# Kernel tuning notes

Measured on AMD Instinct MI355X. Metric: run time of the kernel, lower is better.

Reference implementation:

```python
import jax, jax.numpy as jnp
import numpy as np

N_NODES = 50000
N_EDGES = 800000
N_GRAPHS = 500
IN_DIM, HID, OUT = 128, 64, 10


def setup_inputs() -> dict:
    key = jax.random.key(0)
    ks = jax.random.split(key, 12)
    x = jax.random.normal(ks[0], (N_NODES, IN_DIM), dtype=jnp.float32)
    edge_index = jax.random.randint(ks[1], (2, N_EDGES), 0, N_NODES, dtype=jnp.int32)
    batch = jnp.sort(jax.random.randint(ks[2], (N_NODES,), 0, N_GRAPHS, dtype=jnp.int32))
    def glorot(k, shape):
        lim = np.sqrt(6.0 / (shape[0] + shape[1]))
        return jax.random.uniform(k, shape, jnp.float32, -lim, lim)
    return {
        "x": x, "edge_index": edge_index, "batch": batch,
        "W1": glorot(ks[3], (IN_DIM, HID)), "b1": jnp.zeros((HID,), jnp.float32),
        "W2": glorot(ks[4], (HID, HID)),    "b2": jnp.zeros((HID,), jnp.float32),
        "W3": glorot(ks[5], (HID, HID)),    "b3": jnp.zeros((HID,), jnp.float32),
        "lin_W1": glorot(ks[6], (HID, HID)), "lin_b1": jnp.zeros((HID,), jnp.float32),
        "lin_W2": glorot(ks[7], (HID, OUT)), "lin_b2": jnp.zeros((OUT,), jnp.float32),
    }


def _gcn_conv(x, src, dst, deg_inv_sqrt, W, b):
    # PyG GCNConv: h = x @ W, then sym-normalized scatter-add over edges (self-loops included in src/dst)
    h = x @ W                                   # [N, out]
    norm = deg_inv_sqrt[src] * deg_inv_sqrt[dst]  # [E+N]
    msgs = h[src] * norm[:, None]               # [E+N, out]  (large gathered intermediate)
    out = jax.ops.segment_sum(msgs, dst, num_segments=N_NODES)
    return out + b


def reference(x, edge_index, batch, W1, b1, W2, b2, W3, b3, lin_W1, lin_b1, lin_W2, lin_b2):
    # add self-loops once; degree (with edge weight 1) computed on target nodes
    loops = jnp.arange(N_NODES, dtype=edge_index.dtype)
    src = jnp.concatenate([edge_index[0], loops])
    dst = jnp.concatenate([edge_index[1], loops])
    deg = jax.ops.segment_sum(jnp.ones_like(dst, dtype=x.dtype), dst, num_segments=N_NODES)
    deg_inv_sqrt = jnp.where(deg > 0, jax.lax.rsqrt(jnp.maximum(deg, 1e-12)), 0.0)

    h = jax.nn.relu(_gcn_conv(x, src, dst, deg_inv_sqrt, W1, b1))
    h = jax.nn.relu(_gcn_conv(h, src, dst, deg_inv_sqrt, W2, b2))
    h = jax.nn.relu(_gcn_conv(h, src, dst, deg_inv_sqrt, W3, b3))

    # global mean pool over graphs
    sums = jax.ops.segment_sum(h, batch, num_segments=N_GRAPHS)
    counts = jax.ops.segment_sum(jnp.ones((h.shape[0],), h.dtype), batch, num_segments=N_GRAPHS)
    pooled = sums / jnp.maximum(counts, 1.0)[:, None]  # [G, HID]

    # MLP head (dropout p=0 / eval -> identity)
    logits = jax.nn.relu(pooled @ lin_W1 + lin_b1) @ lin_W2 + lin_b2
    return (logits, jnp.zeros((), x.dtype))
```

## Files before the change

### kernel.cpp

```cpp
#include <hip/hip_runtime.h>
#include <hip/hip_bf16.h>

#define N_NODES 50000
#define N_EDGES 800000
#define N_GRAPHS 500
#define IN_DIM 128
#define HID 64
#define OUT_DIM 10
#define NB_BUCK ((N_NODES + 63) >> 6)
#define NBLK 256
#define BLDT 1024

__device__ __forceinline__ float bf2f(unsigned short u) {
    return __uint_as_float(((unsigned)u) << 16);
}
__device__ __forceinline__ unsigned short f2bf(float f) {
    unsigned x = __float_as_uint(f);
    x += 0x7fffu + ((x >> 16) & 1u);
    return (unsigned short)(x >> 16);
}
__device__ __forceinline__ void acc8(float a[8], uint4 r) {
    a[0] += __uint_as_float(r.x << 16);
    a[1] += __uint_as_float(r.x & 0xffff0000u);
    a[2] += __uint_as_float(r.y << 16);
    a[3] += __uint_as_float(r.y & 0xffff0000u);
    a[4] += __uint_as_float(r.z << 16);
    a[5] += __uint_as_float(r.z & 0xffff0000u);
    a[6] += __uint_as_float(r.w << 16);
    a[7] += __uint_as_float(r.w & 0xffff0000u);
}

__global__ __launch_bounds__(BLDT) void p1_hist_kernel(const int* __restrict__ dst,
                                                       int* __restrict__ bhist, int e, int epb) {
    __shared__ int h[NB_BUCK];
    int tid = threadIdx.x;
    int blk = blockIdx.x;
    for (int i = tid; i < NB_BUCK; i += BLDT) h[i] = 0;
    __syncthreads();
    int e0 = blk * epb;
    int e1 = e0 + epb;
    if (e1 > e) e1 = e;
    int i = e0 + tid * 4;
    for (; i + 3 < e1; i += BLDT * 4) {
        int4 d4 = *(const int4*)&dst[i];
        atomicAdd(&h[d4.x >> 6], 1);
        atomicAdd(&h[d4.y >> 6], 1);
        atomicAdd(&h[d4.z >> 6], 1);
        atomicAdd(&h[d4.w >> 6], 1);
    }
    for (int k = i; k < e1 && k < i + 4; ++k) atomicAdd(&h[dst[k] >> 6], 1);
    __syncthreads();
    for (int j = tid; j < NB_BUCK; j += BLDT) bhist[blk * NB_BUCK + j] = h[j];
}

__global__ __launch_bounds__(NBLK) void scanA_kernel(int* __restrict__ bhist,
                                                     int* __restrict__ bsum) {
    __shared__ int s[NBLK];
    int b = blockIdx.x;
    int t = threadIdx.x;
    int c = bhist[t * NB_BUCK + b];
    s[t] = c;
    __syncthreads();
    for (int off = 1; off < NBLK; off <<= 1) {
        int x = (t >= off) ? s[t - off] : 0;
        __syncthreads();
        s[t] += x;
        __syncthreads();
    }
    bhist[t * NB_BUCK + b] = s[t] - c;
    if (t == NBLK - 1) bsum[b] = s[t];
}

__global__ __launch_bounds__(BLDT) void p2_place_kernel(
    const int* __restrict__ src, const int* __restrict__ dst,
    const int* __restrict__ bsum, const int* __restrict__ base,
    unsigned* __restrict__ pairs, int* __restrict__ bstart, int e, int epb) {
    __shared__ int h[NB_BUCK];
    __shared__ int sb[NB_BUCK];
    __shared__ int ts[BLDT];
    int tid = threadIdx.x;
    int blk = blockIdx.x;
    int i0 = tid << 2;
    int v0 = 0, v1 = 0, v2 = 0, v3 = 0;
    if (i0 < NB_BUCK) v0 = bsum[i0];
    if (i0 + 1 < NB_BUCK) v1 = bsum[i0 + 1];
    if (i0 + 2 < NB_BUCK) v2 = bsum[i0 + 2];
    if (i0 + 3 < NB_BUCK) v3 = bsum[i0 + 3];
    int tsum = v0 + v1 + v2 + v3;
    ts[tid] = tsum;
    for (int i = tid; i < NB_BUCK; i += BLDT) h[i] = 0;
    __syncthreads();
    for (int off = 1; off < BLDT; off <<= 1) {
        int x = (tid >= off) ? ts[tid - off] : 0;
        __syncthreads();
        ts[tid] += x;
        __syncthreads();
    }
    int excl = ts[tid] - tsum;
    int s0 = excl;
    int s1 = s0 + v0;
    int s2 = s1 + v1;
    int s3 = s2 + v2;
    const int* bb = base + blk * NB_BUCK;
    if (i0 < NB_BUCK) sb[i0] = s0 + bb[i0];
    if (i0 + 1 < NB_BUCK) sb[i0 + 1] = s1 + bb[i0 + 1];
    if (i0 + 2 < NB_BUCK) sb[i0 + 2] = s2 + bb[i0 + 2];
    if (i0 + 3 < NB_BUCK) sb[i0 + 3] = s3 + bb[i0 + 3];
    if (blk == 0) {
        if (i0 < NB_BUCK) bstart[i0] = s0;
        if (i0 + 1 < NB_BUCK) bstart[i0 + 1] = s1;
        if (i0 + 2 < NB_BUCK) bstart[i0 + 2] = s2;
        if (i0 + 3 < NB_BUCK) bstart[i0 + 3] = s3;
        if (tid == 0) bstart[NB_BUCK] = e;
    }
    __syncthreads();
    int e0 = blk * epb;
    int e1 = e0 + epb;
    if (e1 > e) e1 = e;
    int i = e0 + tid * 4;
    for (; i + 3 < e1; i += BLDT * 4) {
        int4 d4 = *(const int4*)&dst[i];
        int4 s4 = *(const int4*)&src[i];
        int b0 = d4.x >> 6, b1 = d4.y >> 6, b2 = d4.z >> 6, b3 = d4.w >> 6;
        int r0 = atomicAdd(&h[b0], 1);
        int r1 = atomicAdd(&h[b1], 1);
        int r2 = atomicAdd(&h[b2], 1);
        int r3 = atomicAdd(&h[b3], 1);
        pairs[sb[b0] + r0] = ((unsigned)(d4.x & 63) << 16) | (unsigned)s4.x;
        pairs[sb[b1] + r1] = ((unsigned)(d4.y & 63) << 16) | (unsigned)s4.y;
        pairs[sb[b2] + r2] = ((unsigned)(d4.z & 63) << 16) | (unsigned)s4.z;
        pairs[sb[b3] + r3] = ((unsigned)(d4.w & 63) << 16) | (unsigned)s4.w;
    }
    for (int k = i; k < e1 && k < i + 4; ++k) {
        int d = dst[k];
        int b = d >> 6;
        int r = atomicAdd(&h[b], 1);
        pairs[sb[b] + r] = ((unsigned)(d & 63) << 16) | (unsigned)src[k];
    }
}

__global__ __launch_bounds__(256) void csr_lin1_kernel(
    const unsigned* __restrict__ pairs, const int* __restrict__ bstart,
    int* __restrict__ rs, float* __restrict__ dinv, int* __restrict__ csr_src,
    const float* __restrict__ A, const float* __restrict__ W,
    unsigned short* __restrict__ C, int n) {
    const int K = IN_DIM;
    __shared__ float As[64][K + 4];
    __shared__ float Ws[K][64];
    __shared__ int lcnt[64];
    __shared__ int lcur[64];
    __shared__ float sdinv[64];
    int b = blockIdx.x;
    int tid = threadIdx.x;
    int beg = bstart[b], end = bstart[b + 1];
    if (tid < 64) lcnt[tid] = 0;
    __syncthreads();
    for (int i = beg + tid; i < end; i += 256) atomicAdd(&lcnt[pairs[i] >> 16], 1);
    __syncthreads();
    if (tid < 64) {
        int c = lcnt[tid];
        int v = c;
#pragma unroll
        for (int off = 1; off < 64; off <<= 1) {
            int t = __shfl_up(v, off);
            if (tid >= off) v += t;
        }
        int excl = v - c;
        int node = b * 64 + tid;
        float dv = rsqrtf((float)(c + 1));
        if (node <= n) {
            rs[node] = beg + excl;
            if (node < n) dinv[node] = dv;
        }
        sdinv[tid] = dv;
        lcur[tid] = beg + excl;
    }
    __syncthreads();
    for (int i = beg + tid; i < end; i += 256) {
        unsigned p = pairs[i];
        int slot = atomicAdd(&lcur[p >> 16], 1);
        csr_src[slot] = (int)(p & 0xffffu);
    }

    int block0 = b * 64;
    int rows = n - block0;
    if (rows > 64) rows = 64;

    const float* Abase = A + (size_t)block0 * K;
    int totalA4 = (rows * K) >> 2;
    for (int i4 = tid; i4 < totalA4; i4 += 256) {
        int i = i4 << 2;
        float4 v = *(const float4*)(Abase + i);
        *(float4*)&As[i / K][i % K] = v;
    }
    {
        const float4* Wv = (const float4*)W;
        float4* Wsv = (float4*)&Ws[0][0];
        for (int i = tid; i < K * 16; i += 256) Wsv[i] = Wv[i];
    }
    __syncthreads();

    int tx = tid & 15;
    int ty = tid >> 4;
    float acc[4][4] = {};
#pragma unroll 2
    for (int k = 0; k < K; k += 4) {
        float4 a[4];
#pragma unroll
        for (int i = 0; i < 4; ++i) a[i] = *(const float4*)&As[ty * 4 + i][k];
        float4 w[4];
#pragma unroll
        for (int kk = 0; kk < 4; ++kk) w[kk] = *(const float4*)&Ws[k + kk][tx * 4];
#pragma unroll
        for (int i = 0; i < 4; ++i) {
            float av[4] = {a[i].x, a[i].y, a[i].z, a[i].w};
#pragma unroll
            for (int kk = 0; kk < 4; ++kk) {
                acc[i][0] += av[kk] * w[kk].x;
                acc[i][1] += av[kk] * w[kk].y;
                acc[i][2] += av[kk] * w[kk].z;
                acc[i][3] += av[kk] * w[kk].w;
            }
        }
    }

#pragma unroll
    for (int i = 0; i < 4; ++i) {
        int r = ty * 4 + i;
        if (r < rows) {
            float s = sdinv[r];
            ushort4 v;
            v.x = f2bf(acc[i][0] * s);
            v.y = f2bf(acc[i][1] * s);
            v.z = f2bf(acc[i][2] * s);
            v.w = f2bf(acc[i][3] * s);
            *(ushort4*)&C[(size_t)(block0 + r) * 64 + tx * 4] = v;
        }
    }
}

__global__ __launch_bounds__(256) void linear_bf_kernel(
    const unsigned short* __restrict__ A, const float* __restrict__ W,
    const float* __restrict__ dinv, unsigned short* __restrict__ C, int n) {
    const int K = HID;
    __shared__ float As[64][K + 4];
    __shared__ float Ws[K][64];
    int tid = threadIdx.x;
    int tx = tid & 15;
    int ty = tid >> 4;
    int block0 = blockIdx.x * 64;
    int rows = n - block0;
    if (rows > 64) rows = 64;

    const unsigned short* Abase = A + (size_t)block0 * K;
    int total8 = rows * 8;
    for (int u = tid; u < total8; u += 256) {
        int r = u >> 3;
        int c8 = (u & 7) << 3;
        uint4 raw = *(const uint4*)(Abase + (size_t)r * K + c8);
        float4 a0, a1;
        a0.x = __uint_as_float(raw.x << 16);
        a0.y = __uint_as_float(raw.x & 0xffff0000u);
        a0.z = __uint_as_float(raw.y << 16);
        a0.w = __uint_as_float(raw.y & 0xffff0000u);
        a1.x = __uint_as_float(raw.z << 16);
        a1.y = __uint_as_float(raw.z & 0xffff0000u);
        a1.z = __uint_as_float(raw.w << 16);
        a1.w = __uint_as_float(raw.w & 0xffff0000u);
        *(float4*)&As[r][c8] = a0;
        *(float4*)&As[r][c8 + 4] = a1;
    }
    {
        const float4* Wv = (const float4*)W;
        float4* Wsv = (float4*)&Ws[0][0];
        for (int i = tid; i < K * 16; i += 256) Wsv[i] = Wv[i];
    }
    __syncthreads();

    float acc[4][4] = {};
#pragma unroll 2
    for (int k = 0; k < K; k += 4) {
        float4 a[4];
#pragma unroll
        for (int i = 0; i < 4; ++i) a[i] = *(const float4*)&As[ty * 4 + i][k];
        float4 w[4];
#pragma unroll
        for (int kk = 0; kk < 4; ++kk) w[kk] = *(const float4*)&Ws[k + kk][tx * 4];
#pragma unroll
        for (int i = 0; i < 4; ++i) {
            float av[4] = {a[i].x, a[i].y, a[i].z, a[i].w};
#pragma unroll
            for (int kk = 0; kk < 4; ++kk) {
                acc[i][0] += av[kk] * w[kk].x;
                acc[i][1] += av[kk] * w[kk].y;
                acc[i][2] += av[kk] * w[kk].z;
                acc[i][3] += av[kk] * w[kk].w;
            }
        }
    }

#pragma unroll
    for (int i = 0; i < 4; ++i) {
        int r = ty * 4 + i;
        if (r < rows) {
            float s = dinv[block0 + r];
            ushort4 v;
            v.x = f2bf(acc[i][0] * s);
            v.y = f2bf(acc[i][1] * s);
            v.z = f2bf(acc[i][2] * s);
            v.w = f2bf(acc[i][3] * s);
            *(ushort4*)&C[(size_t)(block0 + r) * 64 + tx * 4] = v;
        }
    }
}

__global__ __launch_bounds__(256) void gather_kernel(
    const unsigned short* __restrict__ hs, const int* __restrict__ rs,
    const int* __restrict__ csr_src, const float* __restrict__ dinv,
    const float* __restrict__ bias, unsigned short* __restrict__ outp, int n) {
    int wave = threadIdx.x >> 6;
    int node = blockIdx.x * 4 + wave;
    if (node >= n) return;
    int lane = threadIdx.x & 63;
    int eg = lane >> 3;
    int f8 = (lane & 7) << 3;
    int beg = rs[node], end = rs[node + 1];
    int len = end - beg;
    int q = (len + 7) >> 3;
    int mb = beg + eg * q;
    int me = mb + q;
    if (me > end) me = end;
    float a[8] = {0.f, 0.f, 0.f, 0.f, 0.f, 0.f, 0.f, 0.f};
    if (eg == 0) {
        uint4 r = *(const uint4*)&hs[(size_t)node * 64 + f8];
        acc8(a, r);
    }
    int j = mb;
    for (; j + 3 < me; j += 4) {
        int s0 = csr_src[j];
        int s1 = csr_src[j + 1];
        int s2 = csr_src[j + 2];
        int s3 = csr_src[j + 3];
        uint4 r0 = *(const uint4*)&hs[(size_t)s0 * 64 + f8];
        uint4 r1 = *(const uint4*)&hs[(size_t)s1 * 64 + f8];
        uint4 r2 = *(const uint4*)&hs[(size_t)s2 * 64 + f8];
        uint4 r3 = *(const uint4*)&hs[(size_t)s3 * 64 + f8];
        acc8(a, r0);
        acc8(a, r1);
        acc8(a, r2);
        acc8(a, r3);
    }
    if (j + 1 < me) {
        int s0 = csr_src[j];
        int s1 = csr_src[j + 1];
        uint4 r0 = *(const uint4*)&hs[(size_t)s0 * 64 + f8];
        uint4 r1 = *(const uint4*)&hs[(size_t)s1 * 64 + f8];
        acc8(a, r0);
        acc8(a, r1);
        j += 2;
    }
    if (j < me) {
        int s0 = csr_src[j];
        uint4 r0 = *(const uint4*)&hs[(size_t)s0 * 64 + f8];
        acc8(a, r0);
    }
#pragma unroll
    for (int k = 0; k < 8; ++k) a[k] += __shfl_xor(a[k], 8);
#pragma unroll
    for (int k = 0; k < 8; ++k) a[k] += __shfl_xor(a[k], 16);
#pragma unroll
    for (int k = 0; k < 8; ++k) a[k] += __shfl_xor(a[k], 32);
    if (eg == 0) {
        float s = dinv[node];
        float4 b0 = *(const float4*)&bias[f8];
        float4 b1 = *(const float4*)&bias[f8 + 4];
        float v0 = fmaxf(a[0] * s + b0.x, 0.f);
        float v1 = fmaxf(a[1] * s + b0.y, 0.f);
        float v2 = fmaxf(a[2] * s + b0.z, 0.f);
        float v3 = fmaxf(a[3] * s + b0.w, 0.f);
        float v4 = fmaxf(a[4] * s + b1.x, 0.f);
        float v5 = fmaxf(a[5] * s + b1.y, 0.f);
        float v6 = fmaxf(a[6] * s + b1.z, 0.f);
        float v7 = fmaxf(a[7] * s + b1.w, 0.f);
        uint4 o;
        o.x = (unsigned)f2bf(v0) | ((unsigned)f2bf(v1) << 16);
        o.y = (unsigned)f2bf(v2) | ((unsigned)f2bf(v3) << 16);
        o.z = (unsigned)f2bf(v4) | ((unsigned)f2bf(v5) << 16);
        o.w = (unsigned)f2bf(v6) | ((unsigned)f2bf(v7) << 16);
        *(uint4*)&outp[(size_t)node * 64 + f8] = o;
    }
}

__device__ __forceinline__ int lower_bound_dev(const int* __restrict__ a, int n, int v) {
    int lo = 0, hi = n;
    while (lo < hi) {
        int m = (lo + hi) >> 1;
        if (a[m] < v) lo = m + 1; else hi = m;
    }
    return lo;
}

__global__ __launch_bounds__(1024) void pool_head_kernel(
    const unsigned short* __restrict__ h, const int* __restrict__ batch,
    const float* __restrict__ W1, const float* __restrict__ b1,
    const float* __restrict__ W2, const float* __restrict__ b2,
    float* __restrict__ out, int nNodes, int nGraphs) {
    __shared__ float psum[16][64];
    __shared__ float p[64];
    __shared__ float t64[64];
    int g = blockIdx.x;
    int tid = threadIdx.x;
    int f = tid & 63;
    int q = tid >> 6;
    int lo = lower_bound_dev(batch, nNodes, g);
    int hi = lower_bound_dev(batch, nNodes, g + 1);
    float sum = 0.0f;
    for (int i = lo + q; i < hi; i += 16) sum += bf2f(h[(size_t)i * 64 + f]);
    psum[q][f] = sum;
    __syncthreads();
    if (tid < 64) {
        float s = 0.0f;
#pragma unroll
        for (int w = 0; w < 16; ++w) s += psum[w][f];
        float inv = 1.0f / fmaxf((float)(hi - lo), 1.0f);
        p[f] = s * inv;
        float acc = b1[f];
#pragma unroll
        for (int k = 0; k < 64; ++k) acc += p[k] * W1[k * 64 + f];
        t64[f] = fmaxf(acc, 0.0f);
        if (f < OUT_DIM) {
            float acc2 = b2[f];
#pragma unroll
            for (int k = 0; k < 64; ++k) acc2 += t64[k] * W2[k * OUT_DIM + f];
            out[g * OUT_DIM + f] = acc2;
        }
        if (g == 0 && f == 0) out[nGraphs * OUT_DIM] = 0.0f;
    }
}

extern "C" void kernel_launch(void* const* d_in, const int* in_sizes, int n_in,
                              void* d_out, int out_size, void* d_ws, size_t ws_size,
                              hipStream_t stream) {
    const float* x      = (const float*)d_in[0];
    const int*   eidx   = (const int*)d_in[1];
    const int*   batch  = (const int*)d_in[2];
    const float* W1     = (const float*)d_in[3];
    const float* b1     = (const float*)d_in[4];
    const float* W2     = (const float*)d_in[5];
    const float* b2     = (const float*)d_in[6];
    const float* W3     = (const float*)d_in[7];
    const float* b3     = (const float*)d_in[8];
    const float* lin_W1 = (const float*)d_in[9];
    const float* lin_b1 = (const float*)d_in[10];
    const float* lin_W2 = (const float*)d_in[11];
    const float* lin_b2 = (const float*)d_in[12];
    float* out = (float*)d_out;

    const int E = in_sizes[1] / 2;
    const int N = N_NODES;
    const int NF = N * HID;
    int epb = (E + NBLK - 1) / NBLK;
    epb = (epb + 7) & ~7;

    const int* src = eidx;
    const int* dst = eidx + E;

    unsigned short* buf1 = (unsigned short*)d_ws;
    unsigned short* buf2 = buf1 + NF;
    float* dinv = (float*)(buf2 + NF);
    int* bhist  = (int*)(dinv + N);
    int* bsum   = bhist + NBLK * NB_BUCK;
    int* bstart = bsum + NB_BUCK;
    int* rs     = bstart + NB_BUCK + 1;
    int* csr_src = rs + N + 1;
    unsigned* pairs = (unsigned*)(csr_src + E);

    const int TILES = (N + 63) / 64;
    const int GBLK = (N + 3) / 4;

    p1_hist_kernel<<<NBLK, BLDT, 0, stream>>>(dst, bhist, E, epb);
    scanA_kernel<<<NB_BUCK, NBLK, 0, stream>>>(bhist, bsum);
    p2_place_kernel<<<NBLK, BLDT, 0, stream>>>(src, dst, bsum, bhist, pairs, bstart, E, epb);

    csr_lin1_kernel<<<TILES, 256, 0, stream>>>(pairs, bstart, rs, dinv, csr_src,
                                               x, W1, buf1, N);
    gather_kernel<<<GBLK, 256, 0, stream>>>(buf1, rs, csr_src, dinv, b1, buf2, N);

    linear_bf_kernel<<<TILES, 256, 0, stream>>>(buf2, W2, dinv, buf1, N);
    gather_kernel<<<GBLK, 256, 0, stream>>>(buf1, rs, csr_src, dinv, b2, buf2, N);

    linear_bf_kernel<<<TILES, 256, 0, stream>>>(buf2, W3, dinv, buf1, N);
    gather_kernel<<<GBLK, 256, 0, stream>>>(buf1, rs, csr_src, dinv, b3, buf2, N);

    pool_head_kernel<<<N_GRAPHS, 1024, 0, stream>>>(buf2, batch, lin_W1, lin_b1, lin_W2, lin_b2,
                                                    out, N, N_GRAPHS);
}
```

Baseline: 244.8 us.

## Fuse neighbor aggregation with following linear layer into one kernel

```diff
diff --git a/kernel.cpp b/kernel.cpp
--- a/kernel.cpp
+++ b/kernel.cpp
@@ -239,44 +239,89 @@
     }
 }
 
-__global__ __launch_bounds__(256) void linear_bf_kernel(
-    const unsigned short* __restrict__ A, const float* __restrict__ W,
-    const float* __restrict__ dinv, unsigned short* __restrict__ C, int n) {
+__global__ __launch_bounds__(256) void gather_lin_kernel(
+    const unsigned short* __restrict__ hs, const int* __restrict__ rs,
+    const int* __restrict__ csr_src, const float* __restrict__ dinv,
+    const float* __restrict__ bias, const float* __restrict__ W,
+    unsigned short* __restrict__ C, int n) {
     const int K = HID;
     __shared__ float As[64][K + 4];
     __shared__ float Ws[K][64];
     int tid = threadIdx.x;
-    int tx = tid & 15;
-    int ty = tid >> 4;
-    int block0 = blockIdx.x * 64;
+    int b = blockIdx.x;
+    int block0 = b * 64;
     int rows = n - block0;
     if (rows > 64) rows = 64;
 
-    const unsigned short* Abase = A + (size_t)block0 * K;
-    int total8 = rows * 8;
-    for (int u = tid; u < total8; u += 256) {
-        int r = u >> 3;
-        int c8 = (u & 7) << 3;
-        uint4 raw = *(const uint4*)(Abase + (size_t)r * K + c8);
-        float4 a0, a1;
-        a0.x = __uint_as_float(raw.x << 16);
-        a0.y = __uint_as_float(raw.x & 0xffff0000u);
-        a0.z = __uint_as_float(raw.y << 16);
-        a0.w = __uint_as_float(raw.y & 0xffff0000u);
-        a1.x = __uint_as_float(raw.z << 16);
-        a1.y = __uint_as_float(raw.z & 0xffff0000u);
-        a1.z = __uint_as_float(raw.w << 16);
-        a1.w = __uint_as_float(raw.w & 0xffff0000u);
-        *(float4*)&As[r][c8] = a0;
-        *(float4*)&As[r][c8 + 4] = a1;
-    }
     {
         const float4* Wv = (const float4*)W;
         float4* Wsv = (float4*)&Ws[0][0];
         for (int i = tid; i < K * 16; i += 256) Wsv[i] = Wv[i];
     }
-    __syncthreads();
-
+
+    int grp = tid >> 3;
+    int lg = tid & 7;
+    int f8 = lg << 3;
+    float4 bb0 = *(const float4*)&bias[f8];
+    float4 bb1 = *(const float4*)&bias[f8 + 4];
+
+    for (int r = grp; r < 64; r += 32) {
+        int node = block0 + r;
+        float a[8] = {0.f, 0.f, 0.f, 0.f, 0.f, 0.f, 0.f, 0.f};
+        if (node < n) {
+            int beg = rs[node], end = rs[node + 1];
+            {
+                uint4 u = *(const uint4*)&hs[(size_t)node * 64 + f8];
+                acc8(a, u);
+            }
+            int j = beg;
+            for (; j + 3 < end; j += 4) {
+                int s0 = csr_src[j];
+                int s1 = csr_src[j + 1];
+                int s2 = csr_src[j + 2];
+                int s3 = csr_src[j + 3];
+                uint4 r0 = *(const uint4*)&hs[(size_t)s0 * 64 + f8];
+                uint4 r1 = *(const uint4*)&hs[(size_t)s1 * 64 + f8];
+                uint4 r2 = *(const uint4*)&hs[(size_t)s2 * 64 + f8];
+                uint4 r3 = *(const uint4*)&hs[(size_t)s3 * 64 + f8];
+                acc8(a, r0);
+                acc8(a, r1);
+                acc8(a, r2);
+                acc8(a, r3);
+            }
+            if (j + 1 < end) {
+                int s0 = csr_src[j];
+                int s1 = csr_src[j + 1];
+                uint4 r0 = *(const uint4*)&hs[(size_t)s0 * 64 + f8];
+                uint4 r1 = *(const uint4*)&hs[(size_t)s1 * 64 + f8];
+                acc8(a, r0);
+                acc8(a, r1);
+                j += 2;
+            }
+            if (j < end) {
+                int s0 = csr_src[j];
+                uint4 r0 = *(const uint4*)&hs[(size_t)s0 * 64 + f8];
+                acc8(a, r0);
+            }
+            float sc = dinv[node];
+            a[0] = fmaxf(a[0] * sc + bb0.x, 0.f);
+            a[1] = fmaxf(a[1] * sc + bb0.y, 0.f);
+            a[2] = fmaxf(a[2] * sc + bb0.z, 0.f);
+            a[3] = fmaxf(a[3] * sc + bb0.w, 0.f);
+            a[4] = fmaxf(a[4] * sc + bb1.x, 0.f);
+            a[5] = fmaxf(a[5] * sc + bb1.y, 0.f);
+            a[6] = fmaxf(a[6] * sc + bb1.z, 0.f);
+            a[7] = fmaxf(a[7] * sc + bb1.w, 0.f);
+        }
+        float4 w0 = {a[0], a[1], a[2], a[3]};
+        float4 w1 = {a[4], a[5], a[6], a[7]};
+        *(float4*)&As[r][f8] = w0;
+        *(float4*)&As[r][f8 + 4] = w1;
+    }
+    __syncthreads();
+
+    int tx = tid & 15;
+    int ty = tid >> 4;
     float acc[4][4] = {};
 #pragma unroll 2
     for (int k = 0; k < K; k += 4) {
@@ -484,12 +529,11 @@
 
     csr_lin1_kernel<<<TILES, 256, 0, stream>>>(pairs, bstart, rs, dinv, csr_src,
                                                x, W1, buf1, N);
-    gather_kernel<<<GBLK, 256, 0, stream>>>(buf1, rs, csr_src, dinv, b1, buf2, N);
-
-    linear_bf_kernel<<<TILES, 256, 0, stream>>>(buf2, W2, dinv, buf1, N);
-    gather_kernel<<<GBLK, 256, 0, stream>>>(buf1, rs, csr_src, dinv, b2, buf2, N);
-
-    linear_bf_kernel<<<TILES, 256, 0, stream>>>(buf2, W3, dinv, buf1, N);
+
+    gather_lin_kernel<<<TILES, 256, 0, stream>>>(buf1, rs, csr_src, dinv, b1, W2, buf2, N);
+
+    gather_lin_kernel<<<TILES, 256, 0, stream>>>(buf2, rs, csr_src, dinv, b2, W3, buf1, N);
+
     gather_kernel<<<GBLK, 256, 0, stream>>>(buf1, rs, csr_src, dinv, b3, buf2, N);
 
     pool_head_kernel<<<N_GRAPHS, 1024, 0, stream>>>(buf2, batch, lin_W1, lin_b1, lin_W2, lin_b2,
```

Result: faster. 219.2 us (-10.5%).
